# Kernel tuning notes

Hardware: AMD Instinct MI355X
Metric: run time of the kernel (lower is better)

## Reference

```python
import itertools
import jax, jax.numpy as jnp
import numpy as np

# --- static configuration (matches init_kwargs) ---
B, O, V = 16, 24, 2            # batch, num_objects, num_total_variables
P0, P1, P2 = 32, 64, 64        # nullary/unary/binary predicate widths
R, C = 3, 16                   # len(arities)=3 ([0,1,2]), num_conjuncts
UI, BI = 1, 2                  # unary_index, binary_index in sorted arities [0,1,2]
NUM_IN = P0 + V * P1 + V * (V - 1) * P2  # 288

# permutation index tables (precomputed constants, as in build())
PERM_IDXS = np.array(list(itertools.permutations(range(O), V)))  # [P, V]
P = PERM_IDXS.shape[0]  # O*(O-1) = 552
_bin_idxs = np.stack(np.nonzero(1 - np.eye(V))).T.reshape(V, V - 1, 2)
_perm_bidxs = PERM_IDXS[:, _bin_idxs]                       # [P, V, V-1, 2]
_shift = (_perm_bidxs[..., 1] > _perm_bidxs[..., 0]).astype(int)
PERM_BIDXS = np.stack([_perm_bidxs[..., 0], _perm_bidxs[..., 1] - _shift], -1)  # [P,V,V-1,2]
BI0 = jnp.asarray(PERM_BIDXS[..., 0])
BI1 = jnp.asarray(PERM_BIDXS[..., 1])


def _probsum(x, axis):
    """Probabilistic OR reduction: 1 - prod(1 - x)."""
    return 1.0 - jnp.prod(1.0 - x, axis=axis)


def setup_inputs() -> dict:
    key = jax.random.key(0)
    k0, k1, k2, k3, k4 = jax.random.split(key, 5)
    return {
        "nullary": jax.random.uniform(k0, (B, P0), dtype=jnp.float32),
        "unary": jax.random.uniform(k1, (B, O, P1), dtype=jnp.float32),
        "binary": jax.random.uniform(k2, (B, O, O - 1, P2), dtype=jnp.float32),
        "and_kernel": 1.0 + 0.1 * jax.random.normal(k3, (R, C, NUM_IN, 3), dtype=jnp.float32),
        "or_kernel": 1.0 + 0.1 * jax.random.normal(k4, (R, C), dtype=jnp.float32),
        "temperature": jnp.ones((), dtype=jnp.float32),
    }


def reference(nullary, unary, binary, and_kernel, or_kernel, temperature):
    # --- compute_permutations ---
    perm_nullary = jnp.broadcast_to(nullary[:, None], (B, P, P0))       # [B,P,P0]
    perm_unary = unary[:, PERM_IDXS]                                    # [B,P,V,P1]
    perm_binary = binary[:, BI0, BI1]                                   # [B,P,V,V-1,P2]
    in_tensor = jnp.concatenate(
        [perm_nullary, perm_unary.reshape(B, P, -1), perm_binary.reshape(B, P, -1)], -1
    )  # [B, P, NUM_IN]

    # --- conjunct (AND) evaluation ---
    ak = jax.nn.softmax(and_kernel / temperature, axis=-1)              # [R,C,NUM_IN,3]
    x = in_tensor[:, :, None, None]                                     # [B,P,1,1,NUM_IN]
    conj_eval = x * ak[..., 0] + (1.0 - x) * ak[..., 1] + ak[..., 2]    # [B,P,R,C,NUM_IN]
    conjuncts = jnp.prod(conj_eval, axis=-1)                            # [B,P,R,C]

    # --- per-arity permutation reductions (OR over unbound variables) ---
    nullary_rules = _probsum(conjuncts[..., :UI, :], axis=1)            # [B,UI,C]
    unary_rules = conjuncts[..., UI:BI, :].reshape(B, O, P // O, BI - UI, C)
    unary_rules = _probsum(unary_rules, axis=2)                         # [B,O,BI-UI,C]
    binary_rules = conjuncts[..., BI:, :].reshape(
        B, O, O - 1, P // (O * (O - 1)), R - BI, C
    )
    binary_rules = _probsum(binary_rules, axis=3)                       # [B,O,O-1,R-BI,C]

    # --- disjunction (OR) over conjuncts ---
    ok = jax.nn.sigmoid(or_kernel / temperature)                        # [R,C]
    nullary_out = _probsum(nullary_rules * ok[:UI], -1)                 # [B,UI]
    unary_out = _probsum(unary_rules * ok[UI:BI], -1)                   # [B,O,BI-UI]
    binary_out = _probsum(binary_rules * ok[BI:], -1)                   # [B,O,O-1,R-BI]
    return nullary_out, unary_out, binary_out
```

## Files before the change

### kernel.cpp

```cpp
#include <hip/hip_runtime.h>
#include <math.h>


#define NBLK_I 72

__device__ __forceinline__ float sigm(float x) { return 1.0f / (1.0f + expf(-x)); }

__global__ __launch_bounds__(256) void prep_kernel(const float* __restrict__ ak,
                                                   const float* __restrict__ temp,
                                                   float* __restrict__ dke) {
    int idx = blockIdx.x * 256 + threadIdx.x;
    if (idx >= 3 * 16 * 288) return;
    int i = idx % 288;
    int c = (idx / 288) % 16;
    int r = idx / (16 * 288);
    float invT = 1.0f / temp[0];
    const float* p = ak + (size_t)idx * 3;
    float a0 = p[0] * invT, a1 = p[1] * invT, a2 = p[2] * invT;
    float mx = fmaxf(a0, fmaxf(a1, a2));
    float e0 = expf(a0 - mx), e1 = expf(a1 - mx), e2 = expf(a2 - mx);
    float inv = 1.0f / (e0 + e1 + e2);
    float s0 = e0 * inv, s1 = e1 * inv, s2 = e2 * inv;
    int ch = i >> 2, lane = i & 3;
    float* q = dke + (((size_t)(ch * 16 + c) * 3 + r) * 8) + lane;
    q[0] = s0 - s1;
    q[4] = s1 + s2;
}

__global__ __launch_bounds__(512) void conj_kernel(const float* __restrict__ nullary,
                                                   const float* __restrict__ unary,
                                                   const float* __restrict__ binary,
                                                   const float* __restrict__ orK,
                                                   const float* __restrict__ temp,
                                                   const float* __restrict__ dke,
                                                   float* __restrict__ out,
                                                   float* __restrict__ ws0) {
    __shared__ float xs[24 * 296];
    __shared__ float part[4][128][9];
    __shared__ float red0[8][16];
    __shared__ float red1[8][16];

    const int tid = threadIdx.x;
    const int blk = blockIdx.x;
    const int b = blk / 24;
    const int a = blk % 24;

    for (int idx = tid; idx < 24 * NBLK_I; idx += 512) {
        int perm = idx / NBLK_I;
        int chunk = idx % NBLK_I;
        int je = perm < 23 ? perm : 22;
        int bb = je + (je >= a ? 1 : 0);
        int aadj = (a > bb) ? (a - 1) : a;
        const float* src;
        if (chunk < 8)        src = nullary + b * 32 + chunk * 4;
        else if (chunk < 24)  src = unary + ((size_t)b * 24 + a) * 64 + (chunk - 8) * 4;
        else if (chunk < 40)  src = unary + ((size_t)b * 24 + bb) * 64 + (chunk - 24) * 4;
        else if (chunk < 56)  src = binary + (((size_t)b * 24 + a) * 23 + je) * 64 + (chunk - 40) * 4;
        else                  src = binary + (((size_t)b * 24 + bb) * 23 + aadj) * 64 + (chunk - 56) * 4;
        float4 v = *(const float4*)src;
        *(float4*)&xs[perm * 296 + chunk * 4] = v;
    }
    __syncthreads();

    const int iq = tid >> 7;
    const int pl = (tid >> 4) & 7;
    const int c  = tid & 15;

    float acc[3][3];
#pragma unroll
    for (int m = 0; m < 3; ++m)
#pragma unroll
        for (int r = 0; r < 3; ++r) acc[m][r] = 1.0f;

    const int ch0 = iq * 18;
#pragma unroll 2
    for (int ch = ch0; ch < ch0 + 18; ++ch) {
        float4 xv[3];
#pragma unroll
        for (int m = 0; m < 3; ++m)
            xv[m] = *(const float4*)&xs[(pl + 8 * m) * 296 + ch * 4];
        const float* kp = dke + (size_t)(ch * 16 + c) * 24;
#pragma unroll
        for (int r = 0; r < 3; ++r) {
            float4 d = *(const float4*)(kp + r * 8);
            float4 e = *(const float4*)(kp + r * 8 + 4);
#pragma unroll
            for (int m = 0; m < 3; ++m) {
                float t0 = fmaf(xv[m].x, d.x, e.x);
                float t1 = fmaf(xv[m].y, d.y, e.y);
                float t2 = fmaf(xv[m].z, d.z, e.z);
                float t3 = fmaf(xv[m].w, d.w, e.w);
                acc[m][r] *= (t0 * t1) * (t2 * t3);
            }
        }
    }

    {
        float* p = part[iq][pl * 16 + c];
#pragma unroll
        for (int m = 0; m < 3; ++m)
#pragma unroll
            for (int r = 0; r < 3; ++r) p[m * 3 + r] = acc[m][r];
    }
    __syncthreads();

    if (iq == 0) {
        const int row = pl * 16 + c;
#pragma unroll
        for (int m = 0; m < 3; ++m)
#pragma unroll
            for (int r = 0; r < 3; ++r)
                acc[m][r] = part[0][row][m * 3 + r] * part[1][row][m * 3 + r]
                          * part[2][row][m * 3 + r] * part[3][row][m * 3 + r];

        const float T = temp[0];
        const float ok2 = sigm(orK[32 + c] / T);

#pragma unroll
        for (int m = 0; m < 3; ++m) {
            int j = pl + 8 * m;
            float w = 1.0f - acc[m][2] * ok2;
#pragma unroll
            for (int off = 1; off < 16; off <<= 1) w *= __shfl_xor(w, off, 16);
            if (c == 0 && j < 23) out[400 + ((size_t)b * 24 + a) * 23 + j] = 1.0f - w;
        }

        float u1 = 1.0f, u0 = 1.0f;
#pragma unroll
        for (int m = 0; m < 3; ++m) {
            int j = pl + 8 * m;
            if (j < 23) {
                u1 *= (1.0f - acc[m][1]);
                u0 *= (1.0f - acc[m][0]);
            }
        }
        red1[pl][c] = u1;
        red0[pl][c] = u0;
    }
    __syncthreads();

    if (tid < 16) {
        int cc = tid;
        float p1 = 1.0f, p0 = 1.0f;
#pragma unroll
        for (int q = 0; q < 8; ++q) { p1 *= red1[q][cc]; p0 *= red0[q][cc]; }
        float T = temp[0];
        float ok1 = sigm(orK[16 + cc] / T);
        float w = 1.0f - (1.0f - p1) * ok1;
#pragma unroll
        for (int off = 1; off < 16; off <<= 1) w *= __shfl_xor(w, off, 16);
        if (cc == 0) out[16 + (size_t)b * 24 + a] = 1.0f - w;
        ws0[((size_t)b * 24 + a) * 16 + cc] = p0;
    }
}

__global__ __launch_bounds__(256) void final_kernel(const float* __restrict__ ws0,
                                                    const float* __restrict__ orK,
                                                    const float* __restrict__ temp,
                                                    float* __restrict__ out) {
    int tid = threadIdx.x;
    int b = tid >> 4, c = tid & 15;
    float p = 1.0f;
#pragma unroll
    for (int a = 0; a < 24; ++a) p *= ws0[((size_t)b * 24 + a) * 16 + c];
    float T = temp[0];
    float ok0 = sigm(orK[c] / T);
    float w = 1.0f - (1.0f - p) * ok0;
#pragma unroll
    for (int off = 1; off < 16; off <<= 1) w *= __shfl_xor(w, off, 16);
    if (c == 0) out[b] = 1.0f - w;
}

extern "C" void kernel_launch(void* const* d_in, const int* in_sizes, int n_in,
                              void* d_out, int out_size, void* d_ws, size_t ws_size,
                              hipStream_t stream) {
    const float* nullary = (const float*)d_in[0];
    const float* unary   = (const float*)d_in[1];
    const float* binary  = (const float*)d_in[2];
    const float* ak      = (const float*)d_in[3];
    const float* orK     = (const float*)d_in[4];
    const float* temp    = (const float*)d_in[5];

    float* out = (float*)d_out;
    float* dke = (float*)d_ws;
    float* ws0 = dke + 27648;

    prep_kernel<<<54, 256, 0, stream>>>(ak, temp, dke);
    conj_kernel<<<16 * 24, 512, 0, stream>>>(nullary, unary, binary, orK, temp, dke, out, ws0);
    final_kernel<<<1, 256, 0, stream>>>(ws0, orK, temp, out);
}
```

Before: 88.31 us.

## Split conjunct product over input halves across twice as many blocks

```diff
diff --git a/kernel.cpp b/kernel.cpp
--- a/kernel.cpp
+++ b/kernel.cpp
@@ -27,38 +27,37 @@
     q[4] = s1 + s2;
 }
 
-__global__ __launch_bounds__(512) void conj_kernel(const float* __restrict__ nullary,
-                                                   const float* __restrict__ unary,
-                                                   const float* __restrict__ binary,
-                                                   const float* __restrict__ orK,
-                                                   const float* __restrict__ temp,
-                                                   const float* __restrict__ dke,
-                                                   float* __restrict__ out,
-                                                   float* __restrict__ ws0) {
-    __shared__ float xs[24 * 296];
+__global__ __launch_bounds__(512) void conj_part(const float* __restrict__ nullary,
+                                                 const float* __restrict__ unary,
+                                                 const float* __restrict__ binary,
+                                                 const float* __restrict__ dke,
+                                                 float* __restrict__ ws1) {
+    __shared__ float xs[24 * 148];
     __shared__ float part[4][128][9];
-    __shared__ float red0[8][16];
-    __shared__ float red1[8][16];
 
     const int tid = threadIdx.x;
     const int blk = blockIdx.x;
-    const int b = blk / 24;
-    const int a = blk % 24;
-
-    for (int idx = tid; idx < 24 * NBLK_I; idx += 512) {
-        int perm = idx / NBLK_I;
-        int chunk = idx % NBLK_I;
+    const int b = blk / 48;
+    const int rem = blk % 48;
+    const int a = rem >> 1;
+    const int q = rem & 1;
+    const int chbase = q * 36;
+
+    for (int idx = tid; idx < 24 * 36; idx += 512) {
+        int perm = idx / 36;
+        int lc = idx % 36;
+        int gc = chbase + lc;
         int je = perm < 23 ? perm : 22;
         int bb = je + (je >= a ? 1 : 0);
         int aadj = (a > bb) ? (a - 1) : a;
         const float* src;
-        if (chunk < 8)        src = nullary + b * 32 + chunk * 4;
-        else if (chunk < 24)  src = unary + ((size_t)b * 24 + a) * 64 + (chunk - 8) * 4;
-        else if (chunk < 40)  src = unary + ((size_t)b * 24 + bb) * 64 + (chunk - 24) * 4;
-        else if (chunk < 56)  src = binary + (((size_t)b * 24 + a) * 23 + je) * 64 + (chunk - 40) * 4;
-        else                  src = binary + (((size_t)b * 24 + bb) * 23 + aadj) * 64 + (chunk - 56) * 4;
+        if (gc < 8)        src = nullary + b * 32 + gc * 4;
+        else if (gc < 24)  src = unary + ((size_t)b * 24 + a) * 64 + (gc - 8) * 4;
+        else if (gc < 40)  src = unary + ((size_t)b * 24 + bb) * 64 + (gc - 24) * 4;
+        else if (gc < 56)  src = binary + (((size_t)b * 24 + a) * 23 + je) * 64 + (gc - 40) * 4;
+        else               src = binary + (((size_t)b * 24 + bb) * 23 + aadj) * 64 + (gc - 56) * 4;
         float4 v = *(const float4*)src;
-        *(float4*)&xs[perm * 296 + chunk * 4] = v;
+        *(float4*)&xs[perm * 148 + lc * 4] = v;
     }
     __syncthreads();
 
@@ -72,14 +71,14 @@
 #pragma unroll
         for (int r = 0; r < 3; ++r) acc[m][r] = 1.0f;
 
-    const int ch0 = iq * 18;
-#pragma unroll 2
-    for (int ch = ch0; ch < ch0 + 18; ++ch) {
+    const int lc0 = iq * 9;
+#pragma unroll 3
+    for (int lc = lc0; lc < lc0 + 9; ++lc) {
         float4 xv[3];
 #pragma unroll
         for (int m = 0; m < 3; ++m)
-            xv[m] = *(const float4*)&xs[(pl + 8 * m) * 296 + ch * 4];
-        const float* kp = dke + (size_t)(ch * 16 + c) * 24;
+            xv[m] = *(const float4*)&xs[(pl + 8 * m) * 148 + lc * 4];
+        const float* kp = dke + (size_t)((chbase + lc) * 16 + c) * 24;
 #pragma unroll
         for (int r = 0; r < 3; ++r) {
             float4 d = *(const float4*)(kp + r * 8);
@@ -106,45 +105,71 @@
 
     if (iq == 0) {
         const int row = pl * 16 + c;
+        float* dst = ws1 + (size_t)blk * 9 * 128;
 #pragma unroll
         for (int m = 0; m < 3; ++m)
 #pragma unroll
             for (int r = 0; r < 3; ++r)
-                acc[m][r] = part[0][row][m * 3 + r] * part[1][row][m * 3 + r]
-                          * part[2][row][m * 3 + r] * part[3][row][m * 3 + r];
-
-        const float T = temp[0];
-        const float ok2 = sigm(orK[32 + c] / T);
-
-#pragma unroll
-        for (int m = 0; m < 3; ++m) {
-            int j = pl + 8 * m;
-            float w = 1.0f - acc[m][2] * ok2;
-#pragma unroll
-            for (int off = 1; off < 16; off <<= 1) w *= __shfl_xor(w, off, 16);
-            if (c == 0 && j < 23) out[400 + ((size_t)b * 24 + a) * 23 + j] = 1.0f - w;
+                dst[(m * 3 + r) * 128 + row] =
+                    part[0][row][m * 3 + r] * part[1][row][m * 3 + r]
+                  * part[2][row][m * 3 + r] * part[3][row][m * 3 + r];
+    }
+}
+
+__global__ __launch_bounds__(128) void combine_kernel(const float* __restrict__ ws1,
+                                                      const float* __restrict__ orK,
+                                                      const float* __restrict__ temp,
+                                                      float* __restrict__ out,
+                                                      float* __restrict__ ws0) {
+    __shared__ float red0[8][16];
+    __shared__ float red1[8][16];
+
+    const int tid = threadIdx.x;
+    const int b = blockIdx.x / 24;
+    const int a = blockIdx.x % 24;
+    const int pl = tid >> 4;
+    const int c = tid & 15;
+
+    const float* s0p = ws1 + ((size_t)(b * 48 + a * 2 + 0) * 9) * 128;
+    const float* s1p = ws1 + ((size_t)(b * 48 + a * 2 + 1) * 9) * 128;
+
+    float acc[3][3];
+#pragma unroll
+    for (int m = 0; m < 3; ++m)
+#pragma unroll
+        for (int r = 0; r < 3; ++r)
+            acc[m][r] = s0p[(m * 3 + r) * 128 + tid] * s1p[(m * 3 + r) * 128 + tid];
+
+    const float T = temp[0];
+    const float ok2 = sigm(orK[32 + c] / T);
+
+#pragma unroll
+    for (int m = 0; m < 3; ++m) {
+        int j = pl + 8 * m;
+        float w = 1.0f - acc[m][2] * ok2;
+#pragma unroll
+        for (int off = 1; off < 16; off <<= 1) w *= __shfl_xor(w, off, 16);
+        if (c == 0 && j < 23) out[400 + ((size_t)b * 24 + a) * 23 + j] = 1.0f - w;
+    }
+
+    float u1 = 1.0f, u0 = 1.0f;
+#pragma unroll
+    for (int m = 0; m < 3; ++m) {
+        int j = pl + 8 * m;
+        if (j < 23) {
+            u1 *= (1.0f - acc[m][1]);
+            u0 *= (1.0f - acc[m][0]);
         }
-
-        float u1 = 1.0f, u0 = 1.0f;
-#pragma unroll
-        for (int m = 0; m < 3; ++m) {
-            int j = pl + 8 * m;
-            if (j < 23) {
-                u1 *= (1.0f - acc[m][1]);
-                u0 *= (1.0f - acc[m][0]);
-            }
-        }
-        red1[pl][c] = u1;
-        red0[pl][c] = u0;
-    }
+    }
+    red1[pl][c] = u1;
+    red0[pl][c] = u0;
     __syncthreads();
 
     if (tid < 16) {
         int cc = tid;
         float p1 = 1.0f, p0 = 1.0f;
 #pragma unroll
-        for (int q = 0; q < 8; ++q) { p1 *= red1[q][cc]; p0 *= red0[q][cc]; }
-        float T = temp[0];
+        for (int qq = 0; qq < 8; ++qq) { p1 *= red1[qq][cc]; p0 *= red0[qq][cc]; }
         float ok1 = sigm(orK[16 + cc] / T);
         float w = 1.0f - (1.0f - p1) * ok1;
 #pragma unroll
@@ -184,8 +209,10 @@
     float* out = (float*)d_out;
     float* dke = (float*)d_ws;
     float* ws0 = dke + 27648;
+    float* ws1 = ws0 + 6144;
 
     prep_kernel<<<54, 256, 0, stream>>>(ak, temp, dke);
-    conj_kernel<<<16 * 24, 512, 0, stream>>>(nullary, unary, binary, orK, temp, dke, out, ws0);
+    conj_part<<<768, 512, 0, stream>>>(nullary, unary, binary, dke, ws1);
+    combine_kernel<<<384, 128, 0, stream>>>(ws1, orK, temp, out, ws0);
     final_kernel<<<1, 256, 0, stream>>>(ws0, orK, temp, out);
 }
```

Result: no change. 88.02 us (-0.3%).
